# Performance work log

Measured on AMD Instinct MI355X. Metric: run time of the kernel, lower is better.

## Reference

```python
import jax, jax.numpy as jnp
import numpy as np

B, L, H, X = 64, 512, 1024, 1024
D = H + X  # 2048


def setup_inputs() -> dict:
    key = jax.random.key(0)
    k = jax.random.split(key, 8)
    h_state = jax.random.normal(k[0], (B, L, H), dtype=jnp.float32)
    x = jax.random.normal(k[1], (B, L, X), dtype=jnp.float32)
    trigger = jax.random.randint(k[2], (B, 1), 0, L, dtype=jnp.int64)
    mask = jax.random.randint(k[3], (B, L), 0, 2, dtype=jnp.int32)
    # Linear params (torch Linear: y = x @ W.T + b)
    sa = 1.0 / np.sqrt(D)
    ss = 1.0 / np.sqrt(H)
    W_a = jax.random.uniform(k[4], (D, D), jnp.float32, -sa, sa)
    b_a = jax.random.uniform(k[5], (D,), jnp.float32, -sa, sa)
    W_s = jax.random.uniform(k[6], (D, H), jnp.float32, -ss, ss)
    b_s = jax.random.uniform(k[7], (D,), jnp.float32, -ss, ss)
    return {"h_state": h_state, "x": x, "W_a": W_a, "b_a": b_a,
            "W_s": W_s, "b_s": b_s, "trigger": trigger, "mask": mask}


def reference(h_state, x, W_a, b_a, W_s, b_s, trigger, mask):
    # a: [B, L, D]
    a = jnp.concatenate((h_state, x), axis=-1)
    # direct gather of the trigger position (replaces one_hot+masked_select)
    trig_a = jnp.take_along_axis(a, trigger[:, :, None], axis=1)  # [B, 1, D]
    s = h_state.sum(axis=1)  # [B, H]
    et = jnp.tanh(jnp.einsum('bld,ed->ble', a, W_a) + b_a
                  + (s @ W_s.T + b_s)[:, None, :])  # [B, L, D]
    et = jnp.where(mask[:, :, None] == 0, jnp.float32(-1e9), et)
    attn = jax.nn.softmax(et, axis=-1)  # softmax over feature dim D (as in source)
    # dropout is identity in eval mode
    out = (trig_a * attn).sum(axis=1)  # [B, D]
    return out
```

## Files before the change

kernel.cpp:

```cpp
#include <hip/hip_runtime.h>
#include <cstdint>

#define B_ 64
#define L_ 512
#define H_ 1024
#define D_ 2048

typedef __attribute__((ext_vector_type(8))) short short8;
typedef __attribute__((ext_vector_type(4))) float f32x4;
typedef unsigned int u32;

static __device__ __forceinline__ float bf2f(u32 lo16) {
    u32 u = lo16 << 16;
    return __builtin_bit_cast(float, u);
}
static __device__ __forceinline__ unsigned short f2bf(float f) {
    u32 u = __builtin_bit_cast(u32, f);
    u += 0x7fffu + ((u >> 16) & 1u);
    return (unsigned short)(u >> 16);
}
static __device__ __forceinline__ u32 pk(float x, float y) {
    return (u32)f2bf(x) | ((u32)f2bf(y) << 16);
}
static __device__ __forceinline__ float fast_pexp(float u) {
    u = fminf(15.f, fmaxf(-15.f, u));
    float ex = __expf(2.f * u);
    float th = (ex - 1.f) / (ex + 1.f);
    return __expf(th);
}
static __device__ __forceinline__ void gload_lds16(const unsigned short* g, unsigned short* l) {
    __builtin_amdgcn_global_load_lds((const __attribute__((address_space(1))) u32*)g,
                                     (__attribute__((address_space(3))) u32*)l, 16, 0, 0);
}

__global__ __launch_bounds__(256) void k_s(const float* __restrict__ h, float* __restrict__ s) {
    int t = blockIdx.x * 256 + threadIdx.x;
    int b = t >> 10, hh = t & 1023;
    const float* p = h + ((size_t)b * L_) * H_ + hh;
    float acc = 0.f;
#pragma unroll 8
    for (int l = 0; l < L_; ++l) acc += p[(size_t)l * H_];
    s[t] = acc;
}

__global__ __launch_bounds__(256) void k_compact(const int* __restrict__ mask,
                                                 const float* __restrict__ ba,
                                                 const float* __restrict__ bs,
                                                 int* __restrict__ ridx,
                                                 int* __restrict__ cnt1,
                                                 float* __restrict__ cnt0,
                                                 float* __restrict__ t2) {
    int b = blockIdx.x;
    __shared__ int sm[L_];
    for (int l = threadIdx.x; l < L_; l += 256) sm[l] = mask[b * L_ + l];
    for (int e = threadIdx.x; e < D_; e += 256) t2[b * D_ + e] = ba[e] + bs[e];
    __syncthreads();
    if (threadIdx.x == 0) {
        int* rb = ridx + b * L_;
        int c = 0;
        for (int l = 0; l < L_; ++l) if (sm[l]) rb[c++] = l;
        int n1 = c;
        int last = (c > 0) ? rb[c - 1] : 0;
        for (; c < L_; ++c) rb[c] = last;
        cnt1[b] = n1;
        cnt0[b] = (float)(L_ - n1);
    }
}

__global__ __launch_bounds__(256) void k_cvtW(const float* __restrict__ Wa,
                                              unsigned short* __restrict__ Wb) {
    int t = blockIdx.x * 256 + threadIdx.x;
    float4 v = ((const float4*)Wa)[t];
    ((uint2*)Wb)[t] = make_uint2(pk(v.x, v.y), pk(v.z, v.w));
}

__global__ __launch_bounds__(256) void k_prep(const float* __restrict__ hs, const float* __restrict__ xx,
                                              const int* __restrict__ ridx, const int* __restrict__ cnt1,
                                              unsigned short* __restrict__ Abf) {
    int j = blockIdx.x;
    int b = blockIdx.y;
    int n1 = cnt1[b];
    if (j >= ((n1 + 255) & ~255)) return;
    int l = ridx[b * L_ + j];
    int t = threadIdx.x;
    size_t rb = ((size_t)(b * L_ + l)) << 10;
    const float* src = (t < 128) ? (hs + rb + t * 8) : (xx + rb + (t - 128) * 8);
    float4 v0 = *(const float4*)src;
    float4 v1 = *(const float4*)(src + 4);
    *(uint4*)(Abf + (((size_t)(b * L_ + j)) << 11) + t * 8) =
        make_uint4(pk(v0.x, v0.y), pk(v0.z, v0.w), pk(v1.x, v1.y), pk(v1.z, v1.w));
}

__global__ __launch_bounds__(256) void k_t2(const float* __restrict__ s, const float* __restrict__ Ws,
                                            float* __restrict__ t2) {
    __shared__ float As[16][64];
    __shared__ float Bs[16][64];
    int n0 = blockIdx.x * 64;
    int ks0 = blockIdx.y * 256;
    int tid = threadIdx.x;
    int tx = tid & 15, ty = tid >> 4;
    int r = tid >> 2, q = tid & 3;
    float acc[4][4] = {};
    for (int k0 = ks0; k0 < ks0 + 256; k0 += 16) {
        float4 av = *(const float4*)(s + (size_t)r * H_ + k0 + q * 4);
        float4 bv = *(const float4*)(Ws + (size_t)(n0 + r) * H_ + k0 + q * 4);
        __syncthreads();
        As[q*4+0][r] = av.x; As[q*4+1][r] = av.y; As[q*4+2][r] = av.z; As[q*4+3][r] = av.w;
        Bs[q*4+0][r] = bv.x; Bs[q*4+1][r] = bv.y; Bs[q*4+2][r] = bv.z; Bs[q*4+3][r] = bv.w;
        __syncthreads();
#pragma unroll
        for (int kk = 0; kk < 16; ++kk) {
            float a_[4], b_[4];
            *(float4*)&a_[0] = *(const float4*)&As[kk][ty * 4];
            *(float4*)&b_[0] = *(const float4*)&Bs[kk][tx * 4];
#pragma unroll
            for (int i = 0; i < 4; ++i)
#pragma unroll
                for (int j = 0; j < 4; ++j) acc[i][j] += a_[i] * b_[j];
        }
    }
#pragma unroll
    for (int i = 0; i < 4; ++i)
#pragma unroll
        for (int j = 0; j < 4; ++j)
            atomicAdd(&t2[(size_t)(ty * 4 + i) * D_ + n0 + tx * 4 + j], acc[i][j]);
}

#define BAR3() do { asm volatile("" ::: "memory"); __builtin_amdgcn_s_barrier(); asm volatile("" ::: "memory"); } while (0)

__global__ __launch_bounds__(512, 2) void k_gemm3(
    const unsigned short* __restrict__ Abf, const unsigned short* __restrict__ Wb,
    const float* __restrict__ t2, const int* __restrict__ cnt1,
    float* __restrict__ rowsum, unsigned short* __restrict__ P)
{
    __shared__ unsigned short lds[65536];

    int tid = threadIdx.x;
    int lane = tid & 63;
    int w = tid >> 6;
    int wm = w >> 2;
    int wn = w & 3;
    int g = lane >> 4;
    int cl = lane & 15;

    int bx = blockIdx.x;
    int jt = ((bx & 7) << 4) | (bx >> 3);
    int n0 = blockIdx.y * 256;
    int b = jt >> 1;
    int j0 = (jt & 1) * 256;
    int n1 = cnt1[b];
    if (j0 >= n1) return;

    int sr = w * 16 + (lane & 15);
    int sce = ((lane >> 4) & 3) * 8;
    const unsigned short* aS0 = Abf + (((size_t)(b * L_ + j0 + sr)) << 11) + sce;
    const unsigned short* aS1 = aS0 + ((size_t)128 << 11);
    const unsigned short* bS0 = Wb + (((size_t)(n0 + sr)) << 11) + sce;
    const unsigned short* bS1 = bS0 + ((size_t)128 << 11);
    int wq = w * 512;

#define STAGE_A3(h, tk, u) do { \
        const unsigned short* s_ = ((h) ? aS1 : aS0) + (tk) * 64; \
        unsigned short* d_ = &lds[(u) * 32768 + (h) * 8192 + wq]; \
        gload_lds16(s_, d_); gload_lds16(s_ + 32, d_ + 4096); } while (0)
#define STAGE_B3(h, tk, u) do { \
        const unsigned short* s_ = ((h) ? bS1 : bS0) + (tk) * 64; \
        unsigned short* d_ = &lds[(u) * 32768 + 16384 + (h) * 8192 + wq]; \
        gload_lds16(s_, d_); gload_lds16(s_ + 32, d_ + 4096); } while (0)

    int rdA = wm * 8192 + g * 128 + cl * 8;
    int rdB = 16384 + (wn >> 1) * 8192 + (wn & 1) * 2048 + g * 128 + cl * 8;

    f32x4 acc[8][4] = {};
    short8 af[4][2], bf0[2][2], bf1[2][2];

    STAGE_A3(0, 0, 0); STAGE_B3(0, 0, 0); STAGE_B3(1, 0, 0); STAGE_A3(1, 0, 0);
    STAGE_B3(0, 1, 1); STAGE_B3(1, 1, 1); STAGE_A3(0, 1, 1);
    asm volatile("s_waitcnt vmcnt(6)" ::: "memory");
    BAR3();

    for (int t = 0; t < 32; ++t) {
        int u = t & 1;
        int ub = u * 32768;
        int tn = (t + 1) & 31, tnn = (t + 2) & 31;

#pragma unroll
        for (int m = 0; m < 4; ++m) {
            af[m][0] = *(const short8*)&lds[ub + rdA + m * 512];
            af[m][1] = *(const short8*)&lds[ub + rdA + 4096 + m * 512];
        }
#pragma unroll
        for (int n = 0; n < 2; ++n) {
            bf0[n][0] = *(const short8*)&lds[ub + rdB + n * 512];
            bf0[n][1] = *(const short8*)&lds[ub + rdB + 4096 + n * 512];
        }
#pragma unroll
        for (int n = 0; n < 2; ++n) {
            bf1[n][0] = *(const short8*)&lds[ub + rdB + (n + 2) * 512];
            bf1[n][1] = *(const short8*)&lds[ub + rdB + 4096 + (n + 2) * 512];
        }
        STAGE_A3(1, tn, u ^ 1);
        BAR3();

        __builtin_amdgcn_s_setprio(1);
#pragma unroll
        for (int h = 0; h < 2; ++h)
#pragma unroll
            for (int m = 0; m < 4; ++m)
#pragma unroll
                for (int n = 0; n < 2; ++n)
                    acc[m][n] = __builtin_amdgcn_mfma_f32_16x16x32_bf16(af[m][h], bf0[n][h], acc[m][n], 0, 0, 0);
#pragma unroll
        for (int h = 0; h < 2; ++h)
#pragma unroll
            for (int m = 0; m < 4; ++m)
#pragma unroll
                for (int n = 0; n < 2; ++n)
                    acc[m][n + 2] = __builtin_amdgcn_mfma_f32_16x16x32_bf16(af[m][h], bf1[n][h], acc[m][n + 2], 0, 0, 0);
        __builtin_amdgcn_s_setprio(0);

        STAGE_B3(0, tnn, u);
        STAGE_B3(1, tnn, u);
        STAGE_A3(0, tnn, u);

#pragma unroll
        for (int m = 0; m < 4; ++m) {
            af[m][0] = *(const short8*)&lds[ub + rdA + (m + 4) * 512];
            af[m][1] = *(const short8*)&lds[ub + rdA + 4096 + (m + 4) * 512];
        }

        __builtin_amdgcn_s_setprio(1);
#pragma unroll
        for (int h = 0; h < 2; ++h)
#pragma unroll
            for (int m = 0; m < 4; ++m)
#pragma unroll
                for (int n = 0; n < 2; ++n)
                    acc[m + 4][n + 2] = __builtin_amdgcn_mfma_f32_16x16x32_bf16(af[m][h], bf1[n][h], acc[m + 4][n + 2], 0, 0, 0);
#pragma unroll
        for (int h = 0; h < 2; ++h)
#pragma unroll
            for (int m = 0; m < 4; ++m)
#pragma unroll
                for (int n = 0; n < 2; ++n)
                    acc[m + 4][n] = __builtin_amdgcn_mfma_f32_16x16x32_bf16(af[m][h], bf0[n][h], acc[m + 4][n], 0, 0, 0);
        __builtin_amdgcn_s_setprio(0);

        asm volatile("s_waitcnt vmcnt(6)" ::: "memory");
        BAR3();
    }
#undef STAGE_A3
#undef STAGE_B3

    asm volatile("s_waitcnt vmcnt(0)" ::: "memory");
    __syncthreads();

    float t2v[4]; int ecol[4];
#pragma unroll
    for (int n = 0; n < 4; ++n) { ecol[n] = n0 + wn * 64 + n * 16 + cl; t2v[n] = t2[b * D_ + ecol[n]]; }
    int orow0 = b * L_ + j0 + wm * 128;
    int qd = g;

    float rs[8][4] = {};
#pragma unroll
    for (int m = 0; m < 8; ++m) {
        int lrowb = m * 16 + qd * 4;
#pragma unroll
        for (int n = 0; n < 4; ++n) {
#pragma unroll
            for (int gg = 0; gg < 4; ++gg) {
                float p = fast_pexp(acc[m][n][gg] + t2v[n]);
                rs[m][gg] += p;
                P[(size_t)(orow0 + lrowb + gg) * D_ + ecol[n]] = f2bf(p);
            }
        }
    }
#pragma unroll
    for (int m = 0; m < 8; ++m)
#pragma unroll
        for (int gg = 0; gg < 4; ++gg) {
            float v = rs[m][gg];
            v += __shfl_xor(v, 1); v += __shfl_xor(v, 2);
            v += __shfl_xor(v, 4); v += __shfl_xor(v, 8);
            rs[m][gg] = v;
        }
    float* red = (float*)lds;
    if (tid < 256) red[tid] = 0.f;
    __syncthreads();
    if (cl == 0) {
#pragma unroll
        for (int m = 0; m < 8; ++m)
#pragma unroll
            for (int gg = 0; gg < 4; ++gg)
                atomicAdd(&red[wm * 128 + m * 16 + qd * 4 + gg], rs[m][gg]);
    }
    __syncthreads();
    if (tid < 256) atomicAdd(&rowsum[b * L_ + j0 + tid], red[tid]);
}

__global__ __launch_bounds__(256) void k_fin2(const unsigned short* __restrict__ P,
                                              const float* __restrict__ rowsum,
                                              const int* __restrict__ cnt1,
                                              const int* __restrict__ trigger,
                                              const float* __restrict__ hs,
                                              const float* __restrict__ xx,
                                              float* __restrict__ out) {
    int b = blockIdx.y;
    __shared__ float iv[L_];
    int n1 = cnt1[b];
    int lceil = (n1 + 127) & ~127;
    for (int j = threadIdx.x; j < L_; j += 256)
        iv[j] = (j < n1) ? 1.f / rowsum[b * L_ + j] : 0.f;
    __syncthreads();
    int e0 = blockIdx.x * 512 + threadIdx.x * 2;
    const unsigned short* Pb = P + (((size_t)b) << 20) + e0;
    float s0 = 0.f, s1 = 0.f;
#pragma unroll 8
    for (int l = 0; l < lceil; ++l) {
        float f = iv[l];
        u32 pv = *(const u32*)(Pb + (((size_t)l) << 11));
        s0 += f * bf2f(pv & 0xffffu);
        s1 += f * bf2f(pv >> 16);
    }
    float base = (float)(L_ - n1) * (1.f / 2048.f);
    int trig = trigger[b];
    size_t tb = ((size_t)(b * L_ + trig)) << 10;
    float ta0 = (e0 < 1024) ? hs[tb + e0] : xx[tb + e0 - 1024];
    float ta1 = (e0 + 1 < 1024) ? hs[tb + e0 + 1] : xx[tb + e0 + 1 - 1024];
    out[b * D_ + e0]     = (s0 + base) * ta0;
    out[b * D_ + e0 + 1] = (s1 + base) * ta1;
}

#define BM 128
#define BN 128
#define BK 32
#define LDK 40
__global__ __launch_bounds__(256) void k_gemm(
    const float* __restrict__ hs, const float* __restrict__ xx,
    const float* __restrict__ Wa, const unsigned short* __restrict__ Wb,
    const float* __restrict__ t2,
    const int* __restrict__ ridx, const int* __restrict__ cnt1,
    float* __restrict__ rowsum,
    unsigned short* __restrict__ P, float* __restrict__ out, int mode)
{
    __shared__ unsigned short Asl[BM][LDK];
    __shared__ unsigned short Bsl[BN][BK];
    __shared__ float red[BM];

    int tid = threadIdx.x;
    int lane = tid & 63;
    int w = tid >> 6;
    int wm = w & 1, wn = w >> 1;

    int n0 = blockIdx.x * BN;
    int jt = blockIdx.y;
    int b = jt >> 2;
    int j0 = (jt & 3) * BM;
    int n1 = cnt1[b];
    if (j0 >= n1) return;

    int r = tid >> 1;
    int koff = (tid & 1) * 16;
    int l = ridx[b * L_ + j0 + r];
    size_t abase = ((size_t)b * L_ + l) * (size_t)H_;
    const float* hrow = hs + abase;
    const float* xrow = xx + abase;
    const float* browf = Wa + (size_t)(n0 + r) * D_;
    const unsigned short* bw0 = Wb ? Wb + (size_t)(n0 + (tid >> 2)) * D_ + (tid & 3) * 8 : nullptr;
    const unsigned short* bw1 = Wb ? Wb + (size_t)(n0 + 64 + (tid >> 2)) * D_ + (tid & 3) * 8 : nullptr;
    unsigned short* bs0 = &Bsl[0][0] + (size_t)tid * 8;
    unsigned short* bs1 = &Bsl[0][0] + (size_t)(tid + 256) * 8;
    bool useWb = (Wb != nullptr);

    f32x4 acc[4][4] = {};

    for (int k0 = 0; k0 < D_; k0 += BK) {
        int k = k0 + koff;
        const float* ap = (k < H_) ? (hrow + k) : (xrow + (k - H_));
        float4 a0 = *(const float4*)(ap);
        float4 a1 = *(const float4*)(ap + 4);
        float4 a2 = *(const float4*)(ap + 8);
        float4 a3 = *(const float4*)(ap + 12);
        uint4 bv0, bv1;
        float4 c0, c1, c2, c3;
        if (useWb) {
            bv0 = *(const uint4*)(bw0 + k0);
            bv1 = *(const uint4*)(bw1 + k0);
        } else {
            const float* bp = browf + k;
            c0 = *(const float4*)(bp);
            c1 = *(const float4*)(bp + 4);
            c2 = *(const float4*)(bp + 8);
            c3 = *(const float4*)(bp + 12);
        }
        __syncthreads();
        *(uint4*)&Asl[r][koff]     = make_uint4(pk(a0.x,a0.y), pk(a0.z,a0.w), pk(a1.x,a1.y), pk(a1.z,a1.w));
        *(uint4*)&Asl[r][koff + 8] = make_uint4(pk(a2.x,a2.y), pk(a2.z,a2.w), pk(a3.x,a3.y), pk(a3.z,a3.w));
        if (useWb) {
            *(uint4*)bs0 = bv0;
            *(uint4*)bs1 = bv1;
        } else {
            *(uint4*)&Bsl[r][koff]     = make_uint4(pk(c0.x,c0.y), pk(c0.z,c0.w), pk(c1.x,c1.y), pk(c1.z,c1.w));
            *(uint4*)&Bsl[r][koff + 8] = make_uint4(pk(c2.x,c2.y), pk(c2.z,c2.w), pk(c3.x,c3.y), pk(c3.z,c3.w));
        }
        __syncthreads();
        int kb = (lane >> 4) * 8;
        short8 af[4], bfg[4];
#pragma unroll
        for (int i = 0; i < 4; ++i) af[i]  = *(const short8*)&Asl[wm*64 + i*16 + (lane & 15)][kb];
#pragma unroll
        for (int j = 0; j < 4; ++j) bfg[j] = *(const short8*)&Bsl[wn*64 + j*16 + (lane & 15)][kb];
#pragma unroll
        for (int i = 0; i < 4; ++i)
#pragma unroll
            for (int j = 0; j < 4; ++j)
                acc[i][j] = __builtin_amdgcn_mfma_f32_16x16x32_bf16(af[i], bfg[j], acc[i][j], 0, 0, 0);
    }

    int cl = lane & 15, qd = lane >> 4;
    float t2v[4]; int ecol[4];
#pragma unroll
    for (int j = 0; j < 4; ++j) { ecol[j] = n0 + wn*64 + j*16 + cl; t2v[j] = t2[b * D_ + ecol[j]]; }
    int orow0 = b * L_ + j0;

    if (mode <= 1) {
        float rs[4][4] = {};
#pragma unroll
        for (int i = 0; i < 4; ++i) {
            int lrowb = wm*64 + i*16 + qd*4;
#pragma unroll
            for (int j = 0; j < 4; ++j) {
#pragma unroll
                for (int g = 0; g < 4; ++g) {
                    float p = fast_pexp(acc[i][j][g] + t2v[j]);
                    rs[i][g] += p;
                    if (mode == 0)
                        P[(size_t)(orow0 + lrowb + g) * D_ + ecol[j]] = f2bf(p);
                }
            }
        }
#pragma unroll
        for (int i = 0; i < 4; ++i)
#pragma unroll
            for (int g = 0; g < 4; ++g) {
                float v = rs[i][g];
                v += __shfl_xor(v, 1); v += __shfl_xor(v, 2);
                v += __shfl_xor(v, 4); v += __shfl_xor(v, 8);
                rs[i][g] = v;
            }
        __syncthreads();
        if (tid < BM) red[tid] = 0.f;
        __syncthreads();
        if (cl == 0) {
#pragma unroll
            for (int i = 0; i < 4; ++i)
#pragma unroll
                for (int g = 0; g < 4; ++g)
                    atomicAdd(&red[wm*64 + i*16 + qd*4 + g], rs[i][g]);
        }
        __syncthreads();
        if (tid < BM) atomicAdd(&rowsum[orow0 + tid], red[tid]);
    } else {
        float inv[4][4];
#pragma unroll
        for (int i = 0; i < 4; ++i)
#pragma unroll
            for (int g = 0; g < 4; ++g) {
                int lrow = wm*64 + i*16 + qd*4 + g;
                inv[i][g] = (j0 + lrow < n1) ? (1.f / rowsum[orow0 + lrow]) : 0.f;
            }
        float cs[4] = {};
#pragma unroll
        for (int i = 0; i < 4; ++i)
#pragma unroll
            for (int j = 0; j < 4; ++j)
#pragma unroll
                for (int g = 0; g < 4; ++g)
                    cs[j] += fast_pexp(acc[i][j][g] + t2v[j]) * inv[i][g];
#pragma unroll
        for (int j = 0; j < 4; ++j) {
            float v = cs[j];
            v += __shfl_xor(v, 16); v += __shfl_xor(v, 32);
            cs[j] = v;
        }
        __syncthreads();
        if (tid < BN) red[tid] = 0.f;
        __syncthreads();
        if (qd == 0) {
#pragma unroll
            for (int j = 0; j < 4; ++j) atomicAdd(&red[wn*64 + j*16 + cl], cs[j]);
        }
        __syncthreads();
        if (tid < BN) atomicAdd(&out[b * D_ + n0 + tid], red[tid]);
    }
}

__global__ __launch_bounds__(256) void k_inv(const int* __restrict__ cnt1,
                                             const float* __restrict__ rowsum,
                                             float* __restrict__ invr) {
    int t = blockIdx.x * 256 + threadIdx.x;
    int b = t >> 9, j = t & 511;
    invr[t] = (j < cnt1[b]) ? (1.f / rowsum[t]) : 0.f;
}

__global__ __launch_bounds__(256) void k_fin(const unsigned short* __restrict__ P,
                                             const float* __restrict__ invr,
                                             const int* __restrict__ cnt1,
                                             float* __restrict__ out) {
    int b = blockIdx.y;
    int lz = blockIdx.z * 128;
    if (lz >= cnt1[b]) return;
    int e0 = blockIdx.x * 512 + threadIdx.x * 2;
    const unsigned short* Pb = P + ((size_t)b * L_ + lz) * D_ + e0;
    const float* ivb = invr + b * L_ + lz;
    float s0 = 0.f, s1 = 0.f;
    for (int l = 0; l < 128; ++l) {
        float iv = ivb[l];
        u32 pv = *(const u32*)(Pb + (size_t)l * D_);
        s0 += iv * bf2f(pv & 0xffffu);
        s1 += iv * bf2f(pv >> 16);
    }
    atomicAdd(&out[b * D_ + e0], s0);
    atomicAdd(&out[b * D_ + e0 + 1], s1);
}

__global__ __launch_bounds__(256) void k_final(
    const float* __restrict__ hs, const float* __restrict__ xx,
    const int* __restrict__ trigger, const float* __restrict__ cnt0,
    float* __restrict__ out) {
    int t = blockIdx.x * 256 + threadIdx.x;
    int b = t >> 11, e = t & 2047;
    int trig = trigger[b];
    size_t base = ((size_t)b * L_ + trig) * 1024;
    float ta = (e < 1024) ? hs[base + e] : xx[base + e - 1024];
    out[t] = (out[t] + cnt0[b] * (1.0f / 2048.0f)) * ta;
}

extern "C" void kernel_launch(void* const* d_in, const int* in_sizes, int n_in,
                              void* d_out, int out_size, void* d_ws, size_t ws_size,
                              hipStream_t stream) {
    const float* hs = (const float*)d_in[0];
    const float* xx = (const float*)d_in[1];
    const float* Wa = (const float*)d_in[2];
    const float* ba = (const float*)d_in[3];
    const float* Ws = (const float*)d_in[4];
    const float* bs = (const float*)d_in[5];
    const int*   trig = (const int*)d_in[6];
    const int*   mask = (const int*)d_in[7];
    float* out = (float*)d_out;

    float* wsf    = (float*)d_ws;
    float* s      = wsf;
    float* t2     = s + 65536;
    float* cnt0   = t2 + 131072;
    float* rowsum = cnt0 + 64;
    float* invr   = rowsum + 32768;
    int*   cnt1   = (int*)(invr + 32768);
    int*   ridx   = cnt1 + 64;
    unsigned short* P   = (unsigned short*)(ridx + 32768);
    unsigned short* Wb  = P + (size_t)B_ * L_ * D_;
    unsigned short* Abf = Wb + (size_t)D_ * D_;

    const size_t BASE_B   = 1180160ull;
    const size_t NEED_P   = BASE_B + 134217728ull;
    const size_t NEED_WB  = NEED_P + 8388608ull;
    const size_t NEED_ALL = NEED_WB + 134217728ull;
    bool haveP   = ws_size >= NEED_P;
    bool haveWb  = ws_size >= NEED_WB;
    bool haveAll = ws_size >= NEED_ALL;

    (void)hipMemsetAsync(rowsum, 0, (size_t)B_ * L_ * sizeof(float), stream);

    k_s      <<<256, 256, 0, stream>>>(hs, s);
    k_compact<<<B_, 256, 0, stream>>>(mask, ba, bs, ridx, cnt1, cnt0, t2);
    k_t2     <<<dim3(32, 4), 256, 0, stream>>>(s, Ws, t2);

    if (haveAll) {
        k_cvtW <<<4096, 256, 0, stream>>>(Wa, Wb);
        k_prep <<<dim3(512, 64), 256, 0, stream>>>(hs, xx, ridx, cnt1, Abf);
        k_gemm3<<<dim3(128, 8), 512, 0, stream>>>(Abf, Wb, t2, cnt1, rowsum, P);
        k_fin2 <<<dim3(4, 64), 256, 0, stream>>>(P, rowsum, cnt1, trig, hs, xx, out);
    } else {
        dim3 grid(D_ / BN, (B_ * L_) / BM);
        const unsigned short* WbArg = haveWb ? Wb : nullptr;
        if (haveWb) k_cvtW<<<4096, 256, 0, stream>>>(Wa, Wb);
        (void)hipMemsetAsync(out, 0, (size_t)B_ * D_ * sizeof(float), stream);
        if (haveP) {
            k_gemm<<<grid, 256, 0, stream>>>(hs, xx, Wa, WbArg, t2, ridx, cnt1, rowsum, P, out, 0);
            k_inv <<<(B_ * L_) / 256, 256, 0, stream>>>(cnt1, rowsum, invr);
            k_fin <<<dim3(4, 64, 4), 256, 0, stream>>>(P, invr, cnt1, out);
        } else {
            k_gemm<<<grid, 256, 0, stream>>>(hs, xx, Wa, WbArg, t2, ridx, cnt1, rowsum, P, out, 1);
            k_gemm<<<grid, 256, 0, stream>>>(hs, xx, Wa, WbArg, t2, ridx, cnt1, rowsum, P, out, 2);
        }
        k_final<<<(B_ * D_) / 256, 256, 0, stream>>>(hs, xx, trig, cnt0, out);
    }
}
```

Before: 728.9 us.

## Pre-swizzle bf16 A and W into tile-contiguous layout for direct LDS loads

The conversion kernels now write the bf16 copies of W_a and the compacted activations in a tiled order that matches the GEMM's per-wave LDS staging pattern. Each wave's global-to-LDS loads then read one contiguous 1 KB chunk instead of 16 strided row segments. This is meant to improve coalescing and cut TLB and cache-line waste in the main GEMM. The fallback path drops its use of the bf16 weight copy and converts W_a on the fly, since the new layout no longer matches that kernel.

```diff
diff --git a/kernel.cpp b/kernel.cpp
--- a/kernel.cpp
+++ b/kernel.cpp
@@ -69,25 +69,45 @@
 
 __global__ __launch_bounds__(256) void k_cvtW(const float* __restrict__ Wa,
                                               unsigned short* __restrict__ Wb) {
-    int t = blockIdx.x * 256 + threadIdx.x;
-    float4 v = ((const float4*)Wa)[t];
-    ((uint2*)Wb)[t] = make_uint2(pk(v.x, v.y), pk(v.z, v.w));
+    int c = blockIdx.x * 256 + threadIdx.x;
+    int p  = c >> 16;
+    int rh = (c >> 15) & 1;
+    int tk = (c >> 10) & 31;
+    int w  = (c >> 7) & 7;
+    int kh = (c >> 6) & 1;
+    int g  = (c >> 4) & 3;
+    int cl = c & 15;
+    int row = p * 256 + rh * 128 + w * 16 + cl;
+    int k = tk * 64 + kh * 32 + g * 8;
+    const float* src = Wa + (size_t)row * D_ + k;
+    float4 v0 = *(const float4*)src;
+    float4 v1 = *(const float4*)(src + 4);
+    *(uint4*)(Wb + (size_t)c * 8) =
+        make_uint4(pk(v0.x, v0.y), pk(v0.z, v0.w), pk(v1.x, v1.y), pk(v1.z, v1.w));
 }
 
 __global__ __launch_bounds__(256) void k_prep(const float* __restrict__ hs, const float* __restrict__ xx,
                                               const int* __restrict__ ridx, const int* __restrict__ cnt1,
                                               unsigned short* __restrict__ Abf) {
-    int j = blockIdx.x;
     int b = blockIdx.y;
     int n1 = cnt1[b];
-    if (j >= ((n1 + 255) & ~255)) return;
+    int lceil = (n1 + 255) & ~255;
+    int c = blockIdx.x * 256 + threadIdx.x;
+    int rh = c >> 15;
+    int tk = (c >> 10) & 31;
+    int w  = (c >> 7) & 7;
+    int kh = (c >> 6) & 1;
+    int g  = (c >> 4) & 3;
+    int cl = c & 15;
+    int j = rh * 128 + w * 16 + cl;
+    if (j >= lceil) return;
     int l = ridx[b * L_ + j];
-    int t = threadIdx.x;
+    int k = tk * 64 + kh * 32 + g * 8;
     size_t rb = ((size_t)(b * L_ + l)) << 10;
-    const float* src = (t < 128) ? (hs + rb + t * 8) : (xx + rb + (t - 128) * 8);
+    const float* src = (k < H_) ? (hs + rb + k) : (xx + rb + (k - H_));
     float4 v0 = *(const float4*)src;
     float4 v1 = *(const float4*)(src + 4);
-    *(uint4*)(Abf + (((size_t)(b * L_ + j)) << 11) + t * 8) =
+    *(uint4*)(Abf + ((size_t)b << 20) + (size_t)c * 8) =
         make_uint4(pk(v0.x, v0.y), pk(v0.z, v0.w), pk(v1.x, v1.y), pk(v1.z, v1.w));
 }
 
@@ -151,22 +171,19 @@
     int n1 = cnt1[b];
     if (j0 >= n1) return;
 
-    int sr = w * 16 + (lane & 15);
-    int sce = ((lane >> 4) & 3) * 8;
-    const unsigned short* aS0 = Abf + (((size_t)(b * L_ + j0 + sr)) << 11) + sce;
-    const unsigned short* aS1 = aS0 + ((size_t)128 << 11);
-    const unsigned short* bS0 = Wb + (((size_t)(n0 + sr)) << 11) + sce;
-    const unsigned short* bS1 = bS0 + ((size_t)128 << 11);
+    const unsigned short* aT = Abf + ((size_t)b << 20) + (size_t)(j0 >> 7) * 262144;
+    const unsigned short* bT = Wb + (size_t)blockIdx.y * 524288;
+    int srcOff = w * 1024 + lane * 8;
     int wq = w * 512;
 
 #define STAGE_A3(h, tk, u) do { \
-        const unsigned short* s_ = ((h) ? aS1 : aS0) + (tk) * 64; \
+        const unsigned short* s_ = aT + (h) * 262144 + (tk) * 8192 + srcOff; \
         unsigned short* d_ = &lds[(u) * 32768 + (h) * 8192 + wq]; \
-        gload_lds16(s_, d_); gload_lds16(s_ + 32, d_ + 4096); } while (0)
+        gload_lds16(s_, d_); gload_lds16(s_ + 512, d_ + 4096); } while (0)
 #define STAGE_B3(h, tk, u) do { \
-        const unsigned short* s_ = ((h) ? bS1 : bS0) + (tk) * 64; \
+        const unsigned short* s_ = bT + (h) * 262144 + (tk) * 8192 + srcOff; \
         unsigned short* d_ = &lds[(u) * 32768 + 16384 + (h) * 8192 + wq]; \
-        gload_lds16(s_, d_); gload_lds16(s_ + 32, d_ + 4096); } while (0)
+        gload_lds16(s_, d_); gload_lds16(s_ + 512, d_ + 4096); } while (0)
 
     int rdA = wm * 8192 + g * 128 + cl * 8;
     int rdB = 16384 + (wn >> 1) * 8192 + (wn & 1) * 2048 + g * 128 + cl * 8;
@@ -366,11 +383,6 @@
     const float* hrow = hs + abase;
     const float* xrow = xx + abase;
     const float* browf = Wa + (size_t)(n0 + r) * D_;
-    const unsigned short* bw0 = Wb ? Wb + (size_t)(n0 + (tid >> 2)) * D_ + (tid & 3) * 8 : nullptr;
-    const unsigned short* bw1 = Wb ? Wb + (size_t)(n0 + 64 + (tid >> 2)) * D_ + (tid & 3) * 8 : nullptr;
-    unsigned short* bs0 = &Bsl[0][0] + (size_t)tid * 8;
-    unsigned short* bs1 = &Bsl[0][0] + (size_t)(tid + 256) * 8;
-    bool useWb = (Wb != nullptr);
 
     f32x4 acc[4][4] = {};
 
@@ -381,28 +393,16 @@
         float4 a1 = *(const float4*)(ap + 4);
         float4 a2 = *(const float4*)(ap + 8);
         float4 a3 = *(const float4*)(ap + 12);
-        uint4 bv0, bv1;
-        float4 c0, c1, c2, c3;
-        if (useWb) {
-            bv0 = *(const uint4*)(bw0 + k0);
-            bv1 = *(const uint4*)(bw1 + k0);
-        } else {
-            const float* bp = browf + k;
-            c0 = *(const float4*)(bp);
-            c1 = *(const float4*)(bp + 4);
-            c2 = *(const float4*)(bp + 8);
-            c3 = *(const float4*)(bp + 12);
-        }
+        const float* bp = browf + k;
+        float4 c0 = *(const float4*)(bp);
+        float4 c1 = *(const float4*)(bp + 4);
+        float4 c2 = *(const float4*)(bp + 8);
+        float4 c3 = *(const float4*)(bp + 12);
         __syncthreads();
         *(uint4*)&Asl[r][koff]     = make_uint4(pk(a0.x,a0.y), pk(a0.z,a0.w), pk(a1.x,a1.y), pk(a1.z,a1.w));
         *(uint4*)&Asl[r][koff + 8] = make_uint4(pk(a2.x,a2.y), pk(a2.z,a2.w), pk(a3.x,a3.y), pk(a3.z,a3.w));
-        if (useWb) {
-            *(uint4*)bs0 = bv0;
-            *(uint4*)bs1 = bv1;
-        } else {
-            *(uint4*)&Bsl[r][koff]     = make_uint4(pk(c0.x,c0.y), pk(c0.z,c0.w), pk(c1.x,c1.y), pk(c1.z,c1.w));
-            *(uint4*)&Bsl[r][koff + 8] = make_uint4(pk(c2.x,c2.y), pk(c2.z,c2.w), pk(c3.x,c3.y), pk(c3.z,c3.w));
-        }
+        *(uint4*)&Bsl[r][koff]     = make_uint4(pk(c0.x,c0.y), pk(c0.z,c0.w), pk(c1.x,c1.y), pk(c1.z,c1.w));
+        *(uint4*)&Bsl[r][koff + 8] = make_uint4(pk(c2.x,c2.y), pk(c2.z,c2.w), pk(c3.x,c3.y), pk(c3.z,c3.w));
         __syncthreads();
         int kb = (lane >> 4) * 8;
         short8 af[4], bfg[4];
@@ -566,7 +566,6 @@
     const size_t NEED_WB  = NEED_P + 8388608ull;
     const size_t NEED_ALL = NEED_WB + 134217728ull;
     bool haveP   = ws_size >= NEED_P;
-    bool haveWb  = ws_size >= NEED_WB;
     bool haveAll = ws_size >= NEED_ALL;
 
     (void)hipMemsetAsync(rowsum, 0, (size_t)B_ * L_ * sizeof(float), stream);
@@ -576,22 +575,20 @@
     k_t2     <<<dim3(32, 4), 256, 0, stream>>>(s, Ws, t2);
 
     if (haveAll) {
-        k_cvtW <<<4096, 256, 0, stream>>>(Wa, Wb);
+        k_cvtW <<<2048, 256, 0, stream>>>(Wa, Wb);
         k_prep <<<dim3(512, 64), 256, 0, stream>>>(hs, xx, ridx, cnt1, Abf);
         k_gemm3<<<dim3(128, 8), 512, 0, stream>>>(Abf, Wb, t2, cnt1, rowsum, P);
         k_fin2 <<<dim3(4, 64), 256, 0, stream>>>(P, rowsum, cnt1, trig, hs, xx, out);
     } else {
         dim3 grid(D_ / BN, (B_ * L_) / BM);
-        const unsigned short* WbArg = haveWb ? Wb : nullptr;
-        if (haveWb) k_cvtW<<<4096, 256, 0, stream>>>(Wa, Wb);
         (void)hipMemsetAsync(out, 0, (size_t)B_ * D_ * sizeof(float), stream);
         if (haveP) {
-            k_gemm<<<grid, 256, 0, stream>>>(hs, xx, Wa, WbArg, t2, ridx, cnt1, rowsum, P, out, 0);
+            k_gemm<<<grid, 256, 0, stream>>>(hs, xx, Wa, nullptr, t2, ridx, cnt1, rowsum, P, out, 0);
             k_inv <<<(B_ * L_) / 256, 256, 0, stream>>>(cnt1, rowsum, invr);
             k_fin <<<dim3(4, 64, 4), 256, 0, stream>>>(P, invr, cnt1, out);
         } else {
-            k_gemm<<<grid, 256, 0, stream>>>(hs, xx, Wa, WbArg, t2, ridx, cnt1, rowsum, P, out, 1);
-            k_gemm<<<grid, 256, 0, stream>>>(hs, xx, Wa, WbArg, t2, ridx, cnt1, rowsum, P, out, 2);
+            k_gemm<<<grid, 256, 0, stream>>>(hs, xx, Wa, nullptr, t2, ridx, cnt1, rowsum, P, out, 1);
+            k_gemm<<<grid, 256, 0, stream>>>(hs, xx, Wa, nullptr, t2, ridx, cnt1, rowsum, P, out, 2);
         }
         k_final<<<(B_ * D_) / 256, 256, 0, stream>>>(hs, xx, trig, cnt0, out);
     }
```

Result: faster. 675.3 us (-7.4%).
